# Performance work log

Hardware: AMD Instinct MI355X
Metric: run time of the kernel (lower is better)

The kernel has to match this reference:

```python
import jax, jax.numpy as jnp
import numpy as np

NUM_ROUTERS = 8
K = 2
IN_DIM = 384
HID = 64
TEMP = 1.0
AUX_COEF = 0.05
EPS = 1e-12


def _l2norm(v, axis=-1):
    n = jnp.sqrt(jnp.sum(v * v, axis=axis, keepdims=True))
    return v / jnp.maximum(n, EPS)


def setup_inputs() -> dict:
    key = jax.random.key(0)
    ks = jax.random.split(key, 10)
    B, E = 8192, 1024
    s = 1.0 / np.sqrt(IN_DIM)
    return {
        "x": jax.random.normal(ks[0], (B, IN_DIM), jnp.float32),
        "reasoning_embeddings": jax.random.normal(ks[1], (E, IN_DIM), jnp.float32),
        "random_num": jax.random.uniform(ks[2], (B, 1), jnp.float32),
        "gate_w": jax.random.normal(ks[3], (IN_DIM, NUM_ROUTERS), jnp.float32) * s,
        "gate_b": jnp.zeros((NUM_ROUTERS,), jnp.float32),
        "Uw": jax.random.normal(ks[4], (NUM_ROUTERS, IN_DIM, HID), jnp.float32) * s,
        "Ub": jnp.zeros((NUM_ROUTERS, HID), jnp.float32),
        "Vw": jax.random.normal(ks[5], (NUM_ROUTERS, IN_DIM, HID), jnp.float32) * s,
        "Vb": jnp.zeros((NUM_ROUTERS, HID), jnp.float32),
    }


def reference(x, reasoning_embeddings, random_num, gate_w, gate_b, Uw, Ub, Vw, Vb):
    B = x.shape[0]
    # gate
    logits = x @ gate_w + gate_b                              # [B, R]
    probs = jax.nn.softmax(logits, axis=-1)
    topk_vals, topk_idxs = jax.lax.top_k(logits, K)           # [B, K]
    topk_mask = jax.nn.one_hot(topk_idxs, NUM_ROUTERS).sum(axis=1)  # [B, R]
    aux_loss = NUM_ROUTERS * (probs.mean(0) * topk_mask.mean(0)).sum() * AUX_COEF

    # all routers, batched (replaces the per-(i,j) python loop)
    xu = _l2norm(jnp.einsum("bd,rdh->rbh", x, Uw) + Ub[:, None, :])          # [R, B, H]
    ev = _l2norm(jnp.einsum("ed,rdh->reh", reasoning_embeddings, Vw) + Vb[:, None, :])  # [R, E, H]
    scores = jnp.einsum("rbh,reh->rbe", xu, ev)               # [R, B, E]
    all_out = jax.nn.softmax(scores / TEMP, axis=-1)          # [R, B, E]

    # gather top-k experts per sample
    all_out_b = jnp.transpose(all_out, (1, 0, 2))             # [B, R, E]
    router_outputs = jnp.take_along_axis(all_out_b, topk_idxs[:, :, None], axis=1)  # [B, K, E]

    gate_weights = jax.nn.softmax(topk_vals, axis=-1)[:, :, None]  # [B, K, 1]
    rea_probs = jnp.sum(router_outputs * gate_weights, axis=1)     # [B, E]

    # categorical sampling via inverse-CDF
    scores_cumsum = jnp.cumsum(rea_probs, axis=1)
    selected_index = jnp.argmax((scores_cumsum > random_num).astype(jnp.float32), axis=1)  # [B]
    log_probs = jnp.log(rea_probs[jnp.arange(B), selected_index])[:, None]  # [B, 1]
    return selected_index, log_probs, aux_loss
```

## Files before the change

### kernel.cpp

```cpp
#include <hip/hip_runtime.h>
#include <math.h>

#define B 8192
#define E 1024
#define D 384
#define H 64
#define R 8
#define NCHUNK 16
#define CHUNK_E 64
#define NPOS 17408
#define NROW 25600

#define WS_CNT    0u
#define WS_CUR    32u
#define WS_PS     64u
#define WS_OFFS   96u
#define WS_TOP2   256u
#define WS_GW     65792u
#define WS_POSM   131328u
#define WS_LIST   196864u
#define WS_EVN    266496u
#define WS_XUN    2363648u
#define WS_C      6820096u
#define WS_BUFA   7934208u
#define WS_BUFB   14487808u

__global__ __launch_bounds__(256) void k_gate(
    const float* __restrict__ x, const float* __restrict__ gate_w,
    const float* __restrict__ gate_b, int2* __restrict__ top2,
    float2* __restrict__ gwv, int* __restrict__ counts, float* __restrict__ ps)
{
  __shared__ __align__(16) float gwT[R * 388];
  __shared__ float psl[R];
  __shared__ int   cl[R];
  int tid = threadIdx.x;
  for (int idx = tid; idx < D * R; idx += 256) {
    int k = idx >> 3, r = idx & 7;
    gwT[r * 388 + k] = gate_w[idx];
  }
  if (tid < R) { psl[tid] = 0.f; cl[tid] = 0; }
  __syncthreads();

  int l = tid & 63;
  int r = tid & 7;
  int b = blockIdx.x * 32 + (tid >> 3);
  float acc = gate_b[r];
  const float4* x4 = (const float4*)(x + (size_t)b * D);
  const float*  gr = gwT + r * 388;
#pragma unroll 4
  for (int q = 0; q < 96; ++q) {
    float4 xv = x4[q];
    float4 gv = *(const float4*)&gr[q * 4];
    acc = fmaf(xv.x, gv.x, acc);
    acc = fmaf(xv.y, gv.y, acc);
    acc = fmaf(xv.z, gv.z, acc);
    acc = fmaf(xv.w, gv.w, acc);
  }
  float lv[R];
#pragma unroll
  for (int rr = 0; rr < R; ++rr) lv[rr] = __shfl(acc, (l & ~7) + rr);
  int i0 = 0; float v0 = lv[0];
#pragma unroll
  for (int rr = 1; rr < R; ++rr) if (lv[rr] > v0) { v0 = lv[rr]; i0 = rr; }
  int i1 = (i0 == 0) ? 1 : 0; float v1 = lv[i1];
#pragma unroll
  for (int rr = 0; rr < R; ++rr)
    if (rr != i0 && lv[rr] > v1) { v1 = lv[rr]; i1 = rr; }
  float se = 0.f;
#pragma unroll
  for (int rr = 0; rr < R; ++rr) se += expf(lv[rr] - v0);
  float p = expf(acc - v0) / se;
  if (r == 0) {
    float e10 = expf(v1 - v0);
    top2[b] = make_int2(i0, i1);
    gwv[b]  = make_float2(1.f / (1.f + e10), e10 / (1.f + e10));
  }
  float pa = p;
  int   ca = (r == i0 ? 1 : 0) + (r == i1 ? 1 : 0);
#pragma unroll
  for (int m = 8; m < 64; m <<= 1) {
    pa += __shfl_xor(pa, m);
    ca += __shfl_xor(ca, m);
  }
  if (l < 8) { atomicAdd(&psl[r], pa); atomicAdd(&cl[r], ca); }
  __syncthreads();
  if (tid < R) { atomicAdd(&ps[tid], psl[tid]); atomicAdd(&counts[tid], cl[tid]); }
}

__global__ __launch_bounds__(256) void k_scatter(
    const int2* __restrict__ top2, const int* __restrict__ counts,
    const float* __restrict__ ps, int* __restrict__ cursors,
    int* __restrict__ list, int2* __restrict__ posmap,
    int* __restrict__ offs_g, float* __restrict__ out_aux)
{
  __shared__ int lc[R];
  __shared__ int lbase[R];
  __shared__ int offs[R];
  int tid = threadIdx.x;
  if (tid < R) lc[tid] = 0;
  __syncthreads();
  if (tid == 0) {
    int o = 0;
    for (int r2 = 0; r2 < R; ++r2) { offs[r2] = o; o += (min(counts[r2], B) + 127) & ~127; }
  }
  __syncthreads();
  int b = min(blockIdx.x * 256 + tid, B - 1);
  int2 t = top2[b];
  t.x &= 7; t.y &= 7;
  int p0 = atomicAdd(&lc[t.x], 1);
  int p1 = atomicAdd(&lc[t.y], 1);
  __syncthreads();
  if (tid < R) lbase[tid] = atomicAdd(&cursors[tid], lc[tid]);
  __syncthreads();
  int i0 = min(offs[t.x] + lbase[t.x] + p0, NPOS - 1);
  int i1 = min(offs[t.y] + lbase[t.y] + p1, NPOS - 1);
  list[i0] = b * 2 + 0;
  list[i1] = b * 2 + 1;
  posmap[b] = make_int2(i0, i1);
  if (blockIdx.x == 0 && tid == 0) {
    float s = 0.f;
    for (int r2 = 0; r2 < R; ++r2) {
      s += (ps[r2] / (float)B) * ((float)min(counts[r2], B) / (float)B);
      offs_g[r2] = offs[r2];
    }
    out_aux[0] = (float)R * s * 0.05f;
  }
}

__global__ __launch_bounds__(256) void k_projgemm(
    const float* __restrict__ re, const float* __restrict__ x,
    const float* __restrict__ Vw, const float* __restrict__ Uw,
    const int* __restrict__ list, const int* __restrict__ counts,
    const int* __restrict__ offs, float* __restrict__ bufA,
    float* __restrict__ bufB)
{
  __shared__ __align__(16) float At[64 * 64];
  __shared__ __align__(16) float Wt[64 * 64];
  int tid = threadIdx.x;
  int bid = blockIdx.x;
  int tile = bid >> 1, ks = bid & 1;
  int rowg0 = tile * 64;

  int srow = tid & 63, kq = tid >> 6;
  const float* Wsrc;
  const float* arow;
  if (tile < 128) {
    Wsrc = Vw + (size_t)(rowg0 >> 10) * (D * H);
    arow = re + (size_t)((rowg0 & 1023) + srow) * D;
  } else {
    int pos0 = rowg0 - 8192;
    int tot = offs[R - 1] + ((min(counts[R - 1], B) + 127) & ~127);
    if (pos0 >= tot) return;
    int r = 0;
    for (int rr = 0; rr < R; ++rr) if (pos0 >= offs[rr]) r = rr;
    Wsrc = Uw + (size_t)r * (D * H);
    int gl = list[min(pos0 + srow, NPOS - 1)];
    gl = min(max(gl, 0), 2 * B - 1);
    arow = x + (size_t)(gl >> 1) * D;
  }

  int tr = tid >> 4, tc = tid & 15;
  float acc[4][4];
#pragma unroll
  for (int i = 0; i < 4; ++i)
#pragma unroll
    for (int j = 0; j < 4; ++j) acc[i][j] = 0.f;

  for (int kt = 0; kt < 3; ++kt) {
    int kb = ks * 192 + kt * 64;
    __syncthreads();
#pragma unroll
    for (int q = 0; q < 4; ++q) {
      float4 v = *(const float4*)&arow[kb + (kq + 4 * q) * 4];
      int k0 = (kq + 4 * q) * 4;
      At[(k0 + 0) * 64 + srow] = v.x;
      At[(k0 + 1) * 64 + srow] = v.y;
      At[(k0 + 2) * 64 + srow] = v.z;
      At[(k0 + 3) * 64 + srow] = v.w;
    }
#pragma unroll
    for (int q = 0; q < 4; ++q) {
      int idx = tid + 256 * q;
      int k = idx >> 4, h4 = idx & 15;
      *(float4*)&Wt[k * 64 + h4 * 4] = *(const float4*)&Wsrc[(size_t)(kb + k) * H + h4 * 4];
    }
    __syncthreads();
#pragma unroll 8
    for (int k = 0; k < 64; ++k) {
      float4 a4 = *(const float4*)&At[k * 64 + tr * 4];
      float4 w4 = *(const float4*)&Wt[k * 64 + tc * 4];
      const float* ap = (const float*)&a4;
      const float* wp = (const float*)&w4;
#pragma unroll
      for (int i = 0; i < 4; ++i)
#pragma unroll
        for (int j = 0; j < 4; ++j) acc[i][j] = fmaf(ap[i], wp[j], acc[i][j]);
    }
  }
  float* dst = (ks ? bufB : bufA) + (size_t)rowg0 * H;
#pragma unroll
  for (int i = 0; i < 4; ++i) {
    float4 o;
    o.x = acc[i][0]; o.y = acc[i][1]; o.z = acc[i][2]; o.w = acc[i][3];
    *(float4*)&dst[(tr * 4 + i) * H + tc * 4] = o;
  }
}

__global__ __launch_bounds__(256) void k_projfin(
    const float* __restrict__ bufA, const float* __restrict__ bufB,
    const float* __restrict__ Vb, const float* __restrict__ Ub,
    const int* __restrict__ offs, float* __restrict__ evnT,
    float* __restrict__ xunP)
{
  int tid = threadIdx.x;
  int lane = tid & 63;
  int row0 = blockIdx.x * 32 + (tid >> 6) * 8;
  bool isE = row0 < 8192;
  int r = 0;
  if (isE) {
    r = row0 >> 10;
  } else {
    int pos = row0 - 8192;
    for (int rr = 0; rr < R; ++rr) if (pos >= offs[rr]) r = rr;
  }
  float bias = isE ? Vb[r * H + lane] : Ub[r * H + lane];
#pragma unroll
  for (int i = 0; i < 8; ++i) {
    int row = row0 + i;
    float s = bufA[(size_t)row * H + lane] + bufB[(size_t)row * H + lane] + bias;
    float ss = s * s;
#pragma unroll
    for (int m = 1; m < 64; m <<= 1) ss += __shfl_xor(ss, m);
    float v = s / fmaxf(sqrtf(ss), 1e-12f);
    if (isE) evnT[(size_t)(r * 64 + lane) * 1024 + (row & 1023)] = v;
    else     xunP[(size_t)(row - 8192) * H + lane] = v;
  }
}

__global__ __launch_bounds__(256) void k_pass1(
    const float* __restrict__ evnT, const float* __restrict__ xunP,
    const int* __restrict__ counts, const int* __restrict__ offs,
    float* __restrict__ C)
{
  __shared__ __align__(16) float Xt[32 * 128];
  __shared__ __align__(16) float Et[32 * 128];
  int tid = threadIdx.x;
  int bid = blockIdx.x;
  int et    = bid & 7;
  int stile = (bid >> 3) & 63;
  int r     = bid >> 9;
  int cnt = min(counts[r], B);
  if (cnt <= 0 || stile * 128 >= cnt) return;
  int off = offs[r] + stile * 128;
  int n = min(128, cnt - stile * 128);
  int ebase = et * 128;

  int sg = tid >> 4, egr = tid & 15;
  float acc[8][8];
#pragma unroll
  for (int i = 0; i < 8; ++i)
#pragma unroll
    for (int j = 0; j < 8; ++j) acc[i][j] = 0.f;

  int srow = tid >> 1, shalf = tid & 1;
  int src = min(srow, n - 1);
  const float4* xsrc = (const float4*)(xunP + (size_t)(off + src) * H);

  for (int kst = 0; kst < 2; ++kst) {
    __syncthreads();
    {
#pragma unroll
      for (int q = 0; q < 4; ++q) {
        float4 v = xsrc[kst * 8 + shalf * 4 + q];
        int hb = shalf * 16 + q * 4;
        Xt[(hb + 0) * 128 + srow] = v.x;
        Xt[(hb + 1) * 128 + srow] = v.y;
        Xt[(hb + 2) * 128 + srow] = v.z;
        Xt[(hb + 3) * 128 + srow] = v.w;
      }
    }
    {
#pragma unroll
      for (int q = 0; q < 4; ++q) {
        int idx = tid + 256 * q;
        int h = idx >> 5, e4 = idx & 31;
        *(float4*)&Et[h * 128 + e4 * 4] =
            *(const float4*)(evnT + (size_t)(r * 64 + kst * 32 + h) * 1024 + ebase + e4 * 4);
      }
    }
    __syncthreads();
#pragma unroll 4
    for (int k = 0; k < 32; ++k) {
      float4 xa = *(const float4*)&Xt[k * 128 + sg * 4];
      float4 xb = *(const float4*)&Xt[k * 128 + 64 + sg * 4];
      float4 ea = *(const float4*)&Et[k * 128 + egr * 4];
      float4 eb = *(const float4*)&Et[k * 128 + 64 + egr * 4];
      const float* pa = (const float*)&xa;
      const float* pb = (const float*)&xb;
      const float* qa = (const float*)&ea;
      const float* qb = (const float*)&eb;
#pragma unroll
      for (int i = 0; i < 4; ++i)
#pragma unroll
        for (int j = 0; j < 4; ++j) {
          acc[i][j]         = fmaf(pa[i], qa[j], acc[i][j]);
          acc[i][j + 4]     = fmaf(pa[i], qb[j], acc[i][j + 4]);
          acc[i + 4][j]     = fmaf(pb[i], qa[j], acc[i + 4][j]);
          acc[i + 4][j + 4] = fmaf(pb[i], qb[j], acc[i + 4][j + 4]);
        }
    }
  }

#pragma unroll
  for (int i = 0; i < 8; ++i) {
    float cA = __expf(acc[i][0]) + __expf(acc[i][1]) + __expf(acc[i][2]) + __expf(acc[i][3]);
    float cB = __expf(acc[i][4]) + __expf(acc[i][5]) + __expf(acc[i][6]) + __expf(acc[i][7]);
#pragma unroll
    for (int m = 1; m < 16; m <<= 1) {
      cA += __shfl_xor(cA, m);
      cB += __shfl_xor(cB, m);
    }
    int s = (i < 4) ? (sg * 4 + i) : (64 + sg * 4 + i - 4);
    if (egr == 0 && s < n) {
      C[(size_t)(off + s) * NCHUNK + et * 2]     = cA;
      C[(size_t)(off + s) * NCHUNK + et * 2 + 1] = cB;
    }
  }
}

__global__ __launch_bounds__(256) void k_pass2(
    const float* __restrict__ evnT, const float* __restrict__ xunP,
    const float* __restrict__ C, const int2* __restrict__ top2,
    const int2* __restrict__ posmap, const float2* __restrict__ gwv,
    const float* __restrict__ rnd, float* __restrict__ out)
{
  int tid = threadIdx.x;
  int lane = tid & 63;
  int b = blockIdx.x * 4 + (tid >> 6);
  if (b >= B) return;
  int2 t2 = top2[b];
  t2.x &= 7; t2.y &= 7;
  int2 pm = posmap[b];
  pm.x = min(max(pm.x, 0), NPOS - 1);
  pm.y = min(max(pm.y, 0), NPOS - 1);
  float2 gw = gwv[b];
  float rv = rnd[b];

  const float4* C04 = (const float4*)(C + (size_t)pm.x * NCHUNK);
  const float4* C14 = (const float4*)(C + (size_t)pm.y * NCHUNK);
  float c0[NCHUNK], c1[NCHUNK];
#pragma unroll
  for (int q = 0; q < 4; ++q) {
    float4 v0 = C04[q], v1 = C14[q];
    c0[q*4+0]=v0.x; c0[q*4+1]=v0.y; c0[q*4+2]=v0.z; c0[q*4+3]=v0.w;
    c1[q*4+0]=v1.x; c1[q*4+1]=v1.y; c1[q*4+2]=v1.z; c1[q*4+3]=v1.w;
  }
  float S0 = 0.f, S1 = 0.f;
#pragma unroll
  for (int j = 0; j < NCHUNK; ++j) { S0 += c0[j]; S1 += c1[j]; }
  float a0 = gw.x / S0, a1 = gw.y / S1;
  int cstar = -1; float prefix = 0.f; float run = 0.f;
#pragma unroll
  for (int j = 0; j < NCHUNK; ++j) {
    float nrun = run + (c0[j] * a0 + c1[j] * a1);
    if (cstar < 0 && nrun > rv) { cstar = j; prefix = run; }
    run = nrun;
  }
  float rtgt = rv;
  if (cstar < 0) { cstar = 0; prefix = 0.f; rtgt = -1.0f; }

  float xu0 = xunP[(size_t)pm.x * H + lane];
  float xu1 = xunP[(size_t)pm.y * H + lane];
  const float* E0 = evnT + (size_t)t2.x * 64 * 1024 + cstar * CHUNK_E + lane;
  const float* E1 = evnT + (size_t)t2.y * 64 * 1024 + cstar * CHUNK_E + lane;
  float d0 = 0.f, d1 = 0.f;
#pragma unroll 16
  for (int h = 0; h < 64; ++h) {
    float w0 = __shfl(xu0, h);
    float w1 = __shfl(xu1, h);
    d0 = fmaf(E0[(size_t)h * 1024], w0, d0);
    d1 = fmaf(E1[(size_t)h * 1024], w1, d1);
  }
  float rea = __expf(d0) * a0 + __expf(d1) * a1;
  float sc = rea;
#pragma unroll
  for (int d = 1; d < 64; d <<= 1) {
    float o = __shfl_up(sc, d);
    if (lane >= d) sc += o;
  }
  float cum = prefix + sc;
  unsigned long long m2 = __ballot(cum > rtgt);
  int estar = (m2 == 0ull) ? 63 : (int)__builtin_ctzll(m2);
  float p = __shfl(rea, estar);
  if (lane == 0) {
    int sel = cstar * CHUNK_E + estar;
    out[b]     = (float)sel;
    out[B + b] = logf(p);
  }
}

extern "C" void kernel_launch(void* const* d_in, const int* in_sizes, int n_in,
                              void* d_out, int out_size, void* d_ws, size_t ws_size,
                              hipStream_t stream)
{
  (void)in_sizes; (void)n_in; (void)out_size; (void)ws_size;
  const float* x      = (const float*)d_in[0];
  const float* re     = (const float*)d_in[1];
  const float* rnd    = (const float*)d_in[2];
  const float* gate_w = (const float*)d_in[3];
  const float* gate_b = (const float*)d_in[4];
  const float* Uw     = (const float*)d_in[5];
  const float* Ub     = (const float*)d_in[6];
  const float* Vw     = (const float*)d_in[7];
  const float* Vb     = (const float*)d_in[8];
  char* ws = (char*)d_ws;
  int*    counts  = (int*)(ws + WS_CNT);
  int*    cursors = (int*)(ws + WS_CUR);
  float*  ps      = (float*)(ws + WS_PS);
  int*    offs    = (int*)(ws + WS_OFFS);
  int2*   top2    = (int2*)(ws + WS_TOP2);
  float2* gwv     = (float2*)(ws + WS_GW);
  int2*   posmap  = (int2*)(ws + WS_POSM);
  int*    list    = (int*)(ws + WS_LIST);
  float*  evnT    = (float*)(ws + WS_EVN);
  float*  xunP    = (float*)(ws + WS_XUN);
  float*  Cc      = (float*)(ws + WS_C);
  float*  bufA    = (float*)(ws + WS_BUFA);
  float*  bufB    = (float*)(ws + WS_BUFB);
  float* out = (float*)d_out;

  hipMemsetAsync(ws, 0, 128, stream);
  k_gate    <<<256,  256, 0, stream>>>(x, gate_w, gate_b, top2, gwv, counts, ps);
  k_scatter <<<32,   256, 0, stream>>>(top2, counts, ps, cursors, list, posmap, offs, out + 2 * B);
  k_projgemm<<<800,  256, 0, stream>>>(re, x, Vw, Uw, list, counts, offs, bufA, bufB);
  k_projfin <<<800,  256, 0, stream>>>(bufA, bufB, Vb, Ub, offs, evnT, xunP);
  k_pass1   <<<4096, 256, 0, stream>>>(evnT, xunP, counts, offs, Cc);
  k_pass2   <<<2048, 256, 0, stream>>>(evnT, xunP, Cc, top2, posmap, gwv, rnd, out);
}
```

Measured before the change: 174.8 us.

## Fuse projection finalize into GEMM and use row-major embeddings in sampling pass

Removes the split-K projection GEMM and its separate finalize kernel. Each tile now runs the full K loop and applies bias and L2 normalization in registers, writing xunP directly and writing normalized expert embeddings in both transposed (via LDS) and row-major layouts. The sampling pass reads the row-major copy with float4 loads per lane and the query vector from shared memory, replacing strided column loads and shuffles. In exchange there is half the GEMM parallelism (400 blocks), one extra embedding buffer write, and a block-wide barrier in pass2.

After: 218.5 us. 25.1% more time.

```diff
diff --git a/kernel.cpp b/kernel.cpp
--- a/kernel.cpp
+++ b/kernel.cpp
@@ -9,7 +9,6 @@
 #define NCHUNK 16
 #define CHUNK_E 64
 #define NPOS 17408
-#define NROW 25600
 
 #define WS_CNT    0u
 #define WS_CUR    32u
@@ -22,8 +21,7 @@
 #define WS_EVN    266496u
 #define WS_XUN    2363648u
 #define WS_C      6820096u
-#define WS_BUFA   7934208u
-#define WS_BUFB   14487808u
+#define WS_EVNN   7934208u
 
 __global__ __launch_bounds__(256) void k_gate(
     const float* __restrict__ x, const float* __restrict__ gate_w,
@@ -130,28 +128,31 @@
 __global__ __launch_bounds__(256) void k_projgemm(
     const float* __restrict__ re, const float* __restrict__ x,
     const float* __restrict__ Vw, const float* __restrict__ Uw,
+    const float* __restrict__ Vb, const float* __restrict__ Ub,
     const int* __restrict__ list, const int* __restrict__ counts,
-    const int* __restrict__ offs, float* __restrict__ bufA,
-    float* __restrict__ bufB)
-{
-  __shared__ __align__(16) float At[64 * 64];
-  __shared__ __align__(16) float Wt[64 * 64];
+    const int* __restrict__ offs, float* __restrict__ evnT,
+    float* __restrict__ evnN, float* __restrict__ xunP)
+{
+  __shared__ __align__(16) float lds[8192];
+  float* At = lds;
+  float* Wt = lds + 4096;
   int tid = threadIdx.x;
-  int bid = blockIdx.x;
-  int tile = bid >> 1, ks = bid & 1;
+  int tile = blockIdx.x;
   int rowg0 = tile * 64;
 
   int srow = tid & 63, kq = tid >> 6;
   const float* Wsrc;
   const float* arow;
-  if (tile < 128) {
-    Wsrc = Vw + (size_t)(rowg0 >> 10) * (D * H);
+  int r = 0;
+  bool isE = (tile < 128);
+  if (isE) {
+    r = rowg0 >> 10;
+    Wsrc = Vw + (size_t)r * (D * H);
     arow = re + (size_t)((rowg0 & 1023) + srow) * D;
   } else {
     int pos0 = rowg0 - 8192;
     int tot = offs[R - 1] + ((min(counts[R - 1], B) + 127) & ~127);
     if (pos0 >= tot) return;
-    int r = 0;
     for (int rr = 0; rr < R; ++rr) if (pos0 >= offs[rr]) r = rr;
     Wsrc = Uw + (size_t)r * (D * H);
     int gl = list[min(pos0 + srow, NPOS - 1)];
@@ -166,8 +167,8 @@
 #pragma unroll
     for (int j = 0; j < 4; ++j) acc[i][j] = 0.f;
 
-  for (int kt = 0; kt < 3; ++kt) {
-    int kb = ks * 192 + kt * 64;
+  for (int kt = 0; kt < 6; ++kt) {
+    int kb = kt * 64;
     __syncthreads();
 #pragma unroll
     for (int q = 0; q < 4; ++q) {
@@ -197,43 +198,59 @@
         for (int j = 0; j < 4; ++j) acc[i][j] = fmaf(ap[i], wp[j], acc[i][j]);
     }
   }
-  float* dst = (ks ? bufB : bufA) + (size_t)rowg0 * H;
+
+  const float* bsrc = (isE ? Vb : Ub) + r * H + tc * 4;
+  float4 bv = *(const float4*)bsrc;
+  float vv[4][4];
+#pragma unroll
+  for (int i = 0; i < 4; ++i) {
+    vv[i][0] = acc[i][0] + bv.x;
+    vv[i][1] = acc[i][1] + bv.y;
+    vv[i][2] = acc[i][2] + bv.z;
+    vv[i][3] = acc[i][3] + bv.w;
+    float ss = vv[i][0] * vv[i][0] + vv[i][1] * vv[i][1]
+             + vv[i][2] * vv[i][2] + vv[i][3] * vv[i][3];
+#pragma unroll
+    for (int m = 1; m < 16; m <<= 1) ss += __shfl_xor(ss, m);
+    float dn = fmaxf(sqrtf(ss), 1e-12f);
+    vv[i][0] /= dn; vv[i][1] /= dn; vv[i][2] /= dn; vv[i][3] /= dn;
+  }
+
+  if (!isE) {
+    int pos0 = rowg0 - 8192;
+#pragma unroll
+    for (int i = 0; i < 4; ++i) {
+      float4 o;
+      o.x = vv[i][0]; o.y = vv[i][1]; o.z = vv[i][2]; o.w = vv[i][3];
+      *(float4*)&xunP[(size_t)(pos0 + tr * 4 + i) * H + tc * 4] = o;
+    }
+    return;
+  }
+
+  int ebase = rowg0 & 1023;
 #pragma unroll
   for (int i = 0; i < 4; ++i) {
     float4 o;
-    o.x = acc[i][0]; o.y = acc[i][1]; o.z = acc[i][2]; o.w = acc[i][3];
-    *(float4*)&dst[(tr * 4 + i) * H + tc * 4] = o;
-  }
-}
-
-__global__ __launch_bounds__(256) void k_projfin(
-    const float* __restrict__ bufA, const float* __restrict__ bufB,
-    const float* __restrict__ Vb, const float* __restrict__ Ub,
-    const int* __restrict__ offs, float* __restrict__ evnT,
-    float* __restrict__ xunP)
-{
-  int tid = threadIdx.x;
-  int lane = tid & 63;
-  int row0 = blockIdx.x * 32 + (tid >> 6) * 8;
-  bool isE = row0 < 8192;
-  int r = 0;
-  if (isE) {
-    r = row0 >> 10;
-  } else {
-    int pos = row0 - 8192;
-    for (int rr = 0; rr < R; ++rr) if (pos >= offs[rr]) r = rr;
-  }
-  float bias = isE ? Vb[r * H + lane] : Ub[r * H + lane];
-#pragma unroll
-  for (int i = 0; i < 8; ++i) {
-    int row = row0 + i;
-    float s = bufA[(size_t)row * H + lane] + bufB[(size_t)row * H + lane] + bias;
-    float ss = s * s;
-#pragma unroll
-    for (int m = 1; m < 64; m <<= 1) ss += __shfl_xor(ss, m);
-    float v = s / fmaxf(sqrtf(ss), 1e-12f);
-    if (isE) evnT[(size_t)(r * 64 + lane) * 1024 + (row & 1023)] = v;
-    else     xunP[(size_t)(row - 8192) * H + lane] = v;
+    o.x = vv[i][0]; o.y = vv[i][1]; o.z = vv[i][2]; o.w = vv[i][3];
+    *(float4*)&evnN[((size_t)r * 1024 + ebase + tr * 4 + i) * H + tc * 4] = o;
+  }
+  __syncthreads();
+#pragma unroll
+  for (int i = 0; i < 4; ++i)
+#pragma unroll
+    for (int j = 0; j < 4; ++j)
+      lds[(tc * 4 + j) * 66 + tr * 4 + i] = vv[i][j];
+  __syncthreads();
+#pragma unroll
+  for (int q = 0; q < 4; ++q) {
+    int idx = tid + 256 * q;
+    int h = idx >> 4, f4 = idx & 15;
+    float4 o;
+    o.x = lds[h * 66 + f4 * 4 + 0];
+    o.y = lds[h * 66 + f4 * 4 + 1];
+    o.z = lds[h * 66 + f4 * 4 + 2];
+    o.w = lds[h * 66 + f4 * 4 + 3];
+    *(float4*)&evnT[(size_t)(r * 64 + h) * 1024 + ebase + f4 * 4] = o;
   }
 }
 
@@ -329,15 +346,16 @@
 }
 
 __global__ __launch_bounds__(256) void k_pass2(
-    const float* __restrict__ evnT, const float* __restrict__ xunP,
+    const float* __restrict__ evnN, const float* __restrict__ xunP,
     const float* __restrict__ C, const int2* __restrict__ top2,
     const int2* __restrict__ posmap, const float2* __restrict__ gwv,
     const float* __restrict__ rnd, float* __restrict__ out)
 {
+  __shared__ __align__(16) float sxu[4][2][64];
   int tid = threadIdx.x;
   int lane = tid & 63;
-  int b = blockIdx.x * 4 + (tid >> 6);
-  if (b >= B) return;
+  int w = tid >> 6;
+  int b = blockIdx.x * 4 + w;
   int2 t2 = top2[b];
   t2.x &= 7; t2.y &= 7;
   int2 pm = posmap[b];
@@ -346,6 +364,9 @@
   float2 gw = gwv[b];
   float rv = rnd[b];
 
+  sxu[w][0][lane] = xunP[(size_t)pm.x * H + lane];
+  sxu[w][1][lane] = xunP[(size_t)pm.y * H + lane];
+
   const float4* C04 = (const float4*)(C + (size_t)pm.x * NCHUNK);
   const float4* C14 = (const float4*)(C + (size_t)pm.y * NCHUNK);
   float c0[NCHUNK], c1[NCHUNK];
@@ -369,17 +390,21 @@
   float rtgt = rv;
   if (cstar < 0) { cstar = 0; prefix = 0.f; rtgt = -1.0f; }
 
-  float xu0 = xunP[(size_t)pm.x * H + lane];
-  float xu1 = xunP[(size_t)pm.y * H + lane];
-  const float* E0 = evnT + (size_t)t2.x * 64 * 1024 + cstar * CHUNK_E + lane;
-  const float* E1 = evnT + (size_t)t2.y * 64 * 1024 + cstar * CHUNK_E + lane;
+  __syncthreads();
+
+  const float4* E0 = (const float4*)(evnN + ((size_t)t2.x * 1024 + cstar * CHUNK_E + lane) * H);
+  const float4* E1 = (const float4*)(evnN + ((size_t)t2.y * 1024 + cstar * CHUNK_E + lane) * H);
+  const float4* x0 = (const float4*)&sxu[w][0][0];
+  const float4* x1 = (const float4*)&sxu[w][1][0];
   float d0 = 0.f, d1 = 0.f;
-#pragma unroll 16
-  for (int h = 0; h < 64; ++h) {
-    float w0 = __shfl(xu0, h);
-    float w1 = __shfl(xu1, h);
-    d0 = fmaf(E0[(size_t)h * 1024], w0, d0);
-    d1 = fmaf(E1[(size_t)h * 1024], w1, d1);
+#pragma unroll
+  for (int q = 0; q < 16; ++q) {
+    float4 e0 = E0[q], e1 = E1[q];
+    float4 w0 = x0[q], w1 = x1[q];
+    d0 = fmaf(e0.x, w0.x, d0); d0 = fmaf(e0.y, w0.y, d0);
+    d0 = fmaf(e0.z, w0.z, d0); d0 = fmaf(e0.w, w0.w, d0);
+    d1 = fmaf(e1.x, w1.x, d1); d1 = fmaf(e1.y, w1.y, d1);
+    d1 = fmaf(e1.z, w1.z, d1); d1 = fmaf(e1.w, w1.w, d1);
   }
   float rea = __expf(d0) * a0 + __expf(d1) * a1;
   float sc = rea;
@@ -425,15 +450,13 @@
   float*  evnT    = (float*)(ws + WS_EVN);
   float*  xunP    = (float*)(ws + WS_XUN);
   float*  Cc      = (float*)(ws + WS_C);
-  float*  bufA    = (float*)(ws + WS_BUFA);
-  float*  bufB    = (float*)(ws + WS_BUFB);
+  float*  evnN    = (float*)(ws + WS_EVNN);
   float* out = (float*)d_out;
 
   hipMemsetAsync(ws, 0, 128, stream);
   k_gate    <<<256,  256, 0, stream>>>(x, gate_w, gate_b, top2, gwv, counts, ps);
   k_scatter <<<32,   256, 0, stream>>>(top2, counts, ps, cursors, list, posmap, offs, out + 2 * B);
-  k_projgemm<<<800,  256, 0, stream>>>(re, x, Vw, Uw, list, counts, offs, bufA, bufB);
-  k_projfin <<<800,  256, 0, stream>>>(bufA, bufB, Vb, Ub, offs, evnT, xunP);
+  k_projgemm<<<400,  256, 0, stream>>>(re, x, Vw, Uw, Vb, Ub, list, counts, offs, evnT, evnN, xunP);
   k_pass1   <<<4096, 256, 0, stream>>>(evnT, xunP, counts, offs, Cc);
-  k_pass2   <<<2048, 256, 0, stream>>>(evnT, xunP, Cc, top2, posmap, gwv, rnd, out);
-}
+  k_pass2   <<<2048, 256, 0, stream>>>(evnN, xunP, Cc, top2, posmap, gwv, rnd, out);
+}
```
